# Kernel optimization log

Measured on AMD Instinct MI355X. Metric: run time of the kernel, lower is better.

Reference implementation:

```python
import jax, jax.numpy as jnp
import numpy as np

N_NODES = 100000
N_EDGES = 1600000
D_IN = 256
D_OUT = 128


def setup_inputs() -> dict:
    key = jax.random.key(0)
    k1, k2, k3, k4, k5 = jax.random.split(key, 5)
    x = jax.random.normal(k1, (N_NODES, D_IN), dtype=jnp.float32)
    # Glorot-uniform weight as in weight_variable_glorot
    init_range = np.sqrt(6.0 / (D_IN + D_OUT))
    W = jax.random.uniform(k2, (D_IN, D_OUT), dtype=jnp.float32,
                           minval=-init_range, maxval=init_range)
    adj_rows = jax.random.randint(k3, (N_EDGES,), 0, N_NODES, dtype=jnp.int32)
    adj_cols = jax.random.randint(k4, (N_EDGES,), 0, N_NODES, dtype=jnp.int32)
    adj_vals = jax.random.uniform(k5, (N_EDGES,), dtype=jnp.float32)
    return {"x": x, "W": W, "adj_rows": adj_rows, "adj_cols": adj_cols,
            "adj_vals": adj_vals}


def reference(x, W, adj_rows, adj_cols, adj_vals):
    # dropout with keep_prob = 1 - 0.0 is the identity -> omitted
    h = x @ W                                    # [N, D_OUT] dense projection
    # sparse (COO) adjacency @ h : out[r] += v * h[c]
    msgs = adj_vals[:, None] * h[adj_cols]       # [E, D_OUT]
    agg = jax.ops.segment_sum(msgs, adj_rows, num_segments=N_NODES)
    return jax.nn.relu(agg)                      # act = tf.nn.relu
```

## Files before the change

### kernel.cpp

```cpp
#include <hip/hip_runtime.h>
#include <hip/hip_bf16.h>

#define N_NODES 100000
#define N_EDGES 1600000
#define D_IN 256
#define D_OUT 128

typedef short bf16x8 __attribute__((ext_vector_type(8)));
typedef float f32x4 __attribute__((ext_vector_type(4)));

__device__ __forceinline__ unsigned short f2bf(float f) {
    unsigned int u = __builtin_bit_cast(unsigned int, f);
    u += 0x7fffu + ((u >> 16) & 1u);
    return (unsigned short)(u >> 16);
}
__device__ __forceinline__ float bf_lo(unsigned int h) {
    return __builtin_bit_cast(float, h << 16);
}
__device__ __forceinline__ float bf_hi(unsigned int h) {
    return __builtin_bit_cast(float, h & 0xffff0000u);
}

__global__ __launch_bounds__(256) void convert_w(const float* __restrict__ W,
                                                 unsigned short* __restrict__ WbT) {
    int i = blockIdx.x * 256 + threadIdx.x;
    int k = i >> 7;
    int n = i & 127;
    WbT[(size_t)n * D_IN + k] = f2bf(W[i]);
}

__global__ __launch_bounds__(256) void gemm_mfma(const float* __restrict__ x,
                                                 const unsigned short* __restrict__ WbT,
                                                 unsigned short* __restrict__ hb) {
    const int wave = threadIdx.x >> 6;
    const int lane = threadIdx.x & 63;
    const int row0 = blockIdx.x * 128 + wave * 32;
    if (row0 >= N_NODES) return;
    const int m = lane & 15;
    const int q = lane >> 4;

    const float* xr0 = x + (size_t)(row0 + m) * D_IN;
    const float* xr1 = x + (size_t)(row0 + 16 + m) * D_IN;

    f32x4 acc[2][8];
#pragma unroll
    for (int h = 0; h < 2; ++h)
#pragma unroll
        for (int nt = 0; nt < 8; ++nt) acc[h][nt] = (f32x4){0.f, 0.f, 0.f, 0.f};

#pragma unroll
    for (int kc = 0; kc < 8; ++kc) {
        const int kb = kc * 32 + q * 8;
        float4 a00 = *(const float4*)(xr0 + kb);
        float4 a01 = *(const float4*)(xr0 + kb + 4);
        float4 a10 = *(const float4*)(xr1 + kb);
        float4 a11 = *(const float4*)(xr1 + kb + 4);
        bf16x8 af0, af1;
        af0[0] = (short)f2bf(a00.x); af0[1] = (short)f2bf(a00.y);
        af0[2] = (short)f2bf(a00.z); af0[3] = (short)f2bf(a00.w);
        af0[4] = (short)f2bf(a01.x); af0[5] = (short)f2bf(a01.y);
        af0[6] = (short)f2bf(a01.z); af0[7] = (short)f2bf(a01.w);
        af1[0] = (short)f2bf(a10.x); af1[1] = (short)f2bf(a10.y);
        af1[2] = (short)f2bf(a10.z); af1[3] = (short)f2bf(a10.w);
        af1[4] = (short)f2bf(a11.x); af1[5] = (short)f2bf(a11.y);
        af1[6] = (short)f2bf(a11.z); af1[7] = (short)f2bf(a11.w);
#pragma unroll
        for (int nt = 0; nt < 8; ++nt) {
            bf16x8 bf = *(const bf16x8*)(WbT + (size_t)(nt * 16 + m) * D_IN + kb);
            acc[0][nt] = __builtin_amdgcn_mfma_f32_16x16x32_bf16(af0, bf, acc[0][nt], 0, 0, 0);
            acc[1][nt] = __builtin_amdgcn_mfma_f32_16x16x32_bf16(af1, bf, acc[1][nt], 0, 0, 0);
        }
    }

#pragma unroll
    for (int h = 0; h < 2; ++h)
#pragma unroll
        for (int nt = 0; nt < 8; ++nt)
#pragma unroll
            for (int r = 0; r < 4; ++r) {
                int grow = row0 + h * 16 + q * 4 + r;
                hb[(size_t)grow * D_OUT + nt * 16 + m] = f2bf(acc[h][nt][r]);
            }
}

__global__ __launch_bounds__(256) void hist_rows(const int* __restrict__ rows,
                                                 int* __restrict__ counts) {
    int i = blockIdx.x * 256 + threadIdx.x;
    if (i < N_EDGES / 4) {
        int4 r = *(const int4*)(rows + i * 4);
        atomicAdd(&counts[r.x], 1);
        atomicAdd(&counts[r.y], 1);
        atomicAdd(&counts[r.z], 1);
        atomicAdd(&counts[r.w], 1);
    }
}

#define SCHUNK 1024
__global__ __launch_bounds__(1024) void scan_reduce(const int* __restrict__ counts,
                                                    int* __restrict__ bsum, int n) {
    __shared__ int ws[16];
    const int t = threadIdx.x, lane = t & 63, wid = t >> 6;
    int i = blockIdx.x * SCHUNK + t;
    int v = (i < n) ? counts[i] : 0;
#pragma unroll
    for (int off = 32; off >= 1; off >>= 1) v += __shfl_down(v, off);
    if (lane == 0) ws[wid] = v;
    __syncthreads();
    if (t == 0) {
        int s = 0;
#pragma unroll
        for (int w = 0; w < 16; ++w) s += ws[w];
        bsum[blockIdx.x] = s;
    }
}

__global__ __launch_bounds__(64) void scan_bsums(int* __restrict__ bsum, int nb) {
    const int lane = threadIdx.x;
    int carry = 0;
    for (int base = 0; base < nb; base += 64) {
        int i = base + lane;
        int v = (i < nb) ? bsum[i] : 0;
        int x = v;
#pragma unroll
        for (int off = 1; off < 64; off <<= 1) {
            int u = __shfl_up(x, off);
            if (lane >= off) x += u;
        }
        if (i < nb) bsum[i] = x - v + carry;
        carry += __shfl(x, 63);
    }
}

__global__ __launch_bounds__(1024) void scan_apply(const int* __restrict__ counts,
                                                   const int* __restrict__ bsum,
                                                   int* __restrict__ ptr,
                                                   int* __restrict__ cursor, int n) {
    __shared__ int wtot[16];
    const int t = threadIdx.x, lane = t & 63, wid = t >> 6;
    int i = blockIdx.x * SCHUNK + t;
    int v = (i < n) ? counts[i] : 0;
    int x = v;
#pragma unroll
    for (int off = 1; off < 64; off <<= 1) {
        int u = __shfl_up(x, off);
        if (lane >= off) x += u;
    }
    if (lane == 63) wtot[wid] = x;
    __syncthreads();
    if (wid == 0) {
        int wv = (lane < 16) ? wtot[lane] : 0;
        int y = wv;
#pragma unroll
        for (int off = 1; off < 16; off <<= 1) {
            int u = __shfl_up(y, off);
            if (lane >= off) y += u;
        }
        if (lane < 16) wtot[lane] = y - wv;
    }
    __syncthreads();
    int excl = (x - v) + wtot[wid] + bsum[blockIdx.x];
    if (i < n) {
        ptr[i] = excl;
        cursor[i] = excl;
        if (i == n - 1) ptr[n] = excl + v;
    }
}

#define NWIN 8
#define ROWS_PER_WIN (N_NODES / NWIN)
#define PERM_SLICES 125
__global__ __launch_bounds__(256) void permute_edges(const int* __restrict__ rows,
                                                     const int* __restrict__ cols,
                                                     const float* __restrict__ vals,
                                                     int* __restrict__ cursor,
                                                     int2* __restrict__ edge_r) {
    const int w     = blockIdx.x & (NWIN - 1);
    const int slice = blockIdx.x >> 3;
    const int lo = w * ROWS_PER_WIN;
    const int hi = lo + ROWS_PER_WIN;
    const int per = (N_EDGES / 4) / PERM_SLICES;
    const int beg = slice * per;
    const int end = beg + per;
    for (int i = beg + (int)threadIdx.x; i < end; i += 256) {
        int4   r = *((const int4*)rows + i);
        int4   c = *((const int4*)cols + i);
        float4 v = *((const float4*)vals + i);
        if (r.x >= lo && r.x < hi) {
            int p = atomicAdd(&cursor[r.x], 1);
            edge_r[p] = make_int2(c.x, __builtin_bit_cast(int, v.x));
        }
        if (r.y >= lo && r.y < hi) {
            int p = atomicAdd(&cursor[r.y], 1);
            edge_r[p] = make_int2(c.y, __builtin_bit_cast(int, v.y));
        }
        if (r.z >= lo && r.z < hi) {
            int p = atomicAdd(&cursor[r.z], 1);
            edge_r[p] = make_int2(c.z, __builtin_bit_cast(int, v.z));
        }
        if (r.w >= lo && r.w < hi) {
            int p = atomicAdd(&cursor[r.w], 1);
            edge_r[p] = make_int2(c.w, __builtin_bit_cast(int, v.w));
        }
    }
}

__global__ __launch_bounds__(256) void gather_rows(const int* __restrict__ ptr,
                                                   const int2* __restrict__ edge_r,
                                                   const unsigned short* __restrict__ hb,
                                                   float* __restrict__ out) {
    int row  = blockIdx.x * 4 + (threadIdx.x >> 6);
    int lane = threadIdx.x & 63;
    if (row >= N_NODES) return;
    int beg = __builtin_amdgcn_readfirstlane(ptr[row]);
    int end = __builtin_amdgcn_readfirstlane(ptr[row + 1]);

    float ax0 = 0.f, ay0 = 0.f, ax1 = 0.f, ay1 = 0.f;
    float ax2 = 0.f, ay2 = 0.f, ax3 = 0.f, ay3 = 0.f;
    int j = beg;
    for (; j + 4 <= end; j += 4) {
        int2 e0 = edge_r[j + 0];
        int2 e1 = edge_r[j + 1];
        int2 e2 = edge_r[j + 2];
        int2 e3 = edge_r[j + 3];
        unsigned int h0 = *(const unsigned int*)(hb + (size_t)e0.x * D_OUT + lane * 2);
        unsigned int h1 = *(const unsigned int*)(hb + (size_t)e1.x * D_OUT + lane * 2);
        unsigned int h2 = *(const unsigned int*)(hb + (size_t)e2.x * D_OUT + lane * 2);
        unsigned int h3 = *(const unsigned int*)(hb + (size_t)e3.x * D_OUT + lane * 2);
        float v0 = __builtin_bit_cast(float, e0.y);
        float v1 = __builtin_bit_cast(float, e1.y);
        float v2 = __builtin_bit_cast(float, e2.y);
        float v3 = __builtin_bit_cast(float, e3.y);
        ax0 = fmaf(v0, bf_lo(h0), ax0); ay0 = fmaf(v0, bf_hi(h0), ay0);
        ax1 = fmaf(v1, bf_lo(h1), ax1); ay1 = fmaf(v1, bf_hi(h1), ay1);
        ax2 = fmaf(v2, bf_lo(h2), ax2); ay2 = fmaf(v2, bf_hi(h2), ay2);
        ax3 = fmaf(v3, bf_lo(h3), ax3); ay3 = fmaf(v3, bf_hi(h3), ay3);
    }
    for (; j < end; ++j) {
        int2 e = edge_r[j];
        unsigned int h = *(const unsigned int*)(hb + (size_t)e.x * D_OUT + lane * 2);
        float v = __builtin_bit_cast(float, e.y);
        ax0 = fmaf(v, bf_lo(h), ax0);
        ay0 = fmaf(v, bf_hi(h), ay0);
    }
    float accx = (ax0 + ax1) + (ax2 + ax3);
    float accy = (ay0 + ay1) + (ay2 + ay3);
    float2 o = make_float2(fmaxf(accx, 0.f), fmaxf(accy, 0.f));
    *(float2*)(out + (size_t)row * D_OUT + lane * 2) = o;
}

extern "C" void kernel_launch(void* const* d_in, const int* in_sizes, int n_in,
                              void* d_out, int out_size, void* d_ws, size_t ws_size,
                              hipStream_t stream) {
    const float* x    = (const float*)d_in[0];
    const float* W    = (const float*)d_in[1];
    const int*   rows = (const int*)d_in[2];
    const int*   cols = (const int*)d_in[3];
    const float* vals = (const float*)d_in[4];
    float* out = (float*)d_out;

    char* ws = (char*)d_ws;
    size_t off = 0;
    unsigned short* hb  = (unsigned short*)(ws + off); off += ((size_t)N_NODES * D_OUT * 2 + 255) & ~(size_t)255;
    unsigned short* WbT = (unsigned short*)(ws + off); off += ((size_t)D_IN * D_OUT * 2 + 255) & ~(size_t)255;
    int*  ptr    = (int*)(ws + off); off += ((size_t)(N_NODES + 1) * 4 + 255) & ~(size_t)255;
    int*  cursor = (int*)(ws + off); off += ((size_t)N_NODES * 4 + 255) & ~(size_t)255;
    int2* edge_r = (int2*)(ws + off); off += ((size_t)N_EDGES * 8 + 255) & ~(size_t)255;
    int*  bsum   = (int*)(ws + off); off += 4096;

    const int nscan = (N_NODES + SCHUNK - 1) / SCHUNK;

    convert_w<<<(D_IN * D_OUT) / 256, 256, 0, stream>>>(W, WbT);
    gemm_mfma<<<(N_NODES + 127) / 128, 256, 0, stream>>>(x, WbT, hb);

    (void)hipMemsetAsync(cursor, 0, (size_t)N_NODES * 4, stream);
    hist_rows<<<(N_EDGES / 4 + 255) / 256, 256, 0, stream>>>(rows, cursor);
    scan_reduce<<<nscan, 1024, 0, stream>>>(cursor, bsum, N_NODES);
    scan_bsums<<<1, 64, 0, stream>>>(bsum, nscan);
    scan_apply<<<nscan, 1024, 0, stream>>>(cursor, bsum, ptr, cursor, N_NODES);
    permute_edges<<<NWIN * PERM_SLICES, 256, 0, stream>>>(rows, cols, vals, cursor, edge_r);

    gather_rows<<<(N_NODES + 3) / 4, 256, 0, stream>>>(ptr, edge_r, hb, out);
}
```

Measured before the change: 419.7 us.

## Fuse histogram into GEMM launch, fold memset and block-sum scan into neighbors

Zeroing of the cursor array moves into the weight-conversion kernel. The row histogram becomes extra blocks of the GEMM launch so both run concurrently, and the block-sum scan is recomputed redundantly in every scan_apply block. Together these remove a memset and two kernel launches. permute_edges now uses twice as many slices and loads cols/vals only for edges that fall in its window, trading vector loads for scattered scalar loads in exchange for less wasted read traffic.

```diff
diff --git a/kernel.cpp b/kernel.cpp
--- a/kernel.cpp
+++ b/kernel.cpp
@@ -22,16 +22,35 @@
 }
 
 __global__ __launch_bounds__(256) void convert_w(const float* __restrict__ W,
-                                                 unsigned short* __restrict__ WbT) {
+                                                 unsigned short* __restrict__ WbT,
+                                                 int* __restrict__ cursor) {
     int i = blockIdx.x * 256 + threadIdx.x;
     int k = i >> 7;
     int n = i & 127;
     WbT[(size_t)n * D_IN + k] = f2bf(W[i]);
-}
-
-__global__ __launch_bounds__(256) void gemm_mfma(const float* __restrict__ x,
+    int z = i * 4;
+    if (z < N_NODES) *(int4*)(cursor + z) = make_int4(0, 0, 0, 0);
+}
+
+#define GEMM_BLOCKS ((N_NODES + 127) / 128)
+#define HIST_BLOCKS ((N_EDGES / 4 + 255) / 256)
+__global__ __launch_bounds__(256) void gemm_hist(const float* __restrict__ x,
                                                  const unsigned short* __restrict__ WbT,
-                                                 unsigned short* __restrict__ hb) {
+                                                 unsigned short* __restrict__ hb,
+                                                 const int* __restrict__ rows,
+                                                 int* __restrict__ counts) {
+    if (blockIdx.x >= GEMM_BLOCKS) {
+        int i = (blockIdx.x - GEMM_BLOCKS) * 256 + threadIdx.x;
+        if (i < N_EDGES / 4) {
+            int4 r = *(const int4*)(rows + i * 4);
+            atomicAdd(&counts[r.x], 1);
+            atomicAdd(&counts[r.y], 1);
+            atomicAdd(&counts[r.z], 1);
+            atomicAdd(&counts[r.w], 1);
+        }
+        return;
+    }
+
     const int wave = threadIdx.x >> 6;
     const int lane = threadIdx.x & 63;
     const int row0 = blockIdx.x * 128 + wave * 32;
@@ -83,19 +102,8 @@
             }
 }
 
-__global__ __launch_bounds__(256) void hist_rows(const int* __restrict__ rows,
-                                                 int* __restrict__ counts) {
-    int i = blockIdx.x * 256 + threadIdx.x;
-    if (i < N_EDGES / 4) {
-        int4 r = *(const int4*)(rows + i * 4);
-        atomicAdd(&counts[r.x], 1);
-        atomicAdd(&counts[r.y], 1);
-        atomicAdd(&counts[r.z], 1);
-        atomicAdd(&counts[r.w], 1);
-    }
-}
-
 #define SCHUNK 1024
+#define NSCAN ((N_NODES + SCHUNK - 1) / SCHUNK)
 __global__ __launch_bounds__(1024) void scan_reduce(const int* __restrict__ counts,
                                                     int* __restrict__ bsum, int n) {
     __shared__ int ws[16];
@@ -114,28 +122,12 @@
     }
 }
 
-__global__ __launch_bounds__(64) void scan_bsums(int* __restrict__ bsum, int nb) {
-    const int lane = threadIdx.x;
-    int carry = 0;
-    for (int base = 0; base < nb; base += 64) {
-        int i = base + lane;
-        int v = (i < nb) ? bsum[i] : 0;
-        int x = v;
-#pragma unroll
-        for (int off = 1; off < 64; off <<= 1) {
-            int u = __shfl_up(x, off);
-            if (lane >= off) x += u;
-        }
-        if (i < nb) bsum[i] = x - v + carry;
-        carry += __shfl(x, 63);
-    }
-}
-
 __global__ __launch_bounds__(1024) void scan_apply(const int* __restrict__ counts,
                                                    const int* __restrict__ bsum,
                                                    int* __restrict__ ptr,
-                                                   int* __restrict__ cursor, int n) {
+                                                   int* __restrict__ cursor, int n, int nb) {
     __shared__ int wtot[16];
+    __shared__ int bpre[128];
     const int t = threadIdx.x, lane = t & 63, wid = t >> 6;
     int i = blockIdx.x * SCHUNK + t;
     int v = (i < n) ? counts[i] : 0;
@@ -146,6 +138,22 @@
         if (lane >= off) x += u;
     }
     if (lane == 63) wtot[wid] = x;
+
+    if (wid == 0) {
+        int carry = 0;
+        for (int base = 0; base < nb; base += 64) {
+            int idx = base + lane;
+            int bv = (idx < nb) ? bsum[idx] : 0;
+            int bx = bv;
+#pragma unroll
+            for (int off = 1; off < 64; off <<= 1) {
+                int u = __shfl_up(bx, off);
+                if (lane >= off) bx += u;
+            }
+            if (idx < nb) bpre[idx] = bx - bv + carry;
+            carry += __shfl(bx, 63);
+        }
+    }
     __syncthreads();
     if (wid == 0) {
         int wv = (lane < 16) ? wtot[lane] : 0;
@@ -158,7 +166,7 @@
         if (lane < 16) wtot[lane] = y - wv;
     }
     __syncthreads();
-    int excl = (x - v) + wtot[wid] + bsum[blockIdx.x];
+    int excl = (x - v) + wtot[wid] + bpre[blockIdx.x];
     if (i < n) {
         ptr[i] = excl;
         cursor[i] = excl;
@@ -168,7 +176,7 @@
 
 #define NWIN 8
 #define ROWS_PER_WIN (N_NODES / NWIN)
-#define PERM_SLICES 125
+#define PERM_SLICES 250
 __global__ __launch_bounds__(256) void permute_edges(const int* __restrict__ rows,
                                                      const int* __restrict__ cols,
                                                      const float* __restrict__ vals,
@@ -182,24 +190,23 @@
     const int beg = slice * per;
     const int end = beg + per;
     for (int i = beg + (int)threadIdx.x; i < end; i += 256) {
-        int4   r = *((const int4*)rows + i);
-        int4   c = *((const int4*)cols + i);
-        float4 v = *((const float4*)vals + i);
+        int4 r = *((const int4*)rows + i);
+        const int e = i * 4;
         if (r.x >= lo && r.x < hi) {
             int p = atomicAdd(&cursor[r.x], 1);
-            edge_r[p] = make_int2(c.x, __builtin_bit_cast(int, v.x));
+            edge_r[p] = make_int2(cols[e + 0], __builtin_bit_cast(int, vals[e + 0]));
         }
         if (r.y >= lo && r.y < hi) {
             int p = atomicAdd(&cursor[r.y], 1);
-            edge_r[p] = make_int2(c.y, __builtin_bit_cast(int, v.y));
+            edge_r[p] = make_int2(cols[e + 1], __builtin_bit_cast(int, vals[e + 1]));
         }
         if (r.z >= lo && r.z < hi) {
             int p = atomicAdd(&cursor[r.z], 1);
-            edge_r[p] = make_int2(c.z, __builtin_bit_cast(int, v.z));
+            edge_r[p] = make_int2(cols[e + 2], __builtin_bit_cast(int, vals[e + 2]));
         }
         if (r.w >= lo && r.w < hi) {
             int p = atomicAdd(&cursor[r.w], 1);
-            edge_r[p] = make_int2(c.w, __builtin_bit_cast(int, v.w));
+            edge_r[p] = make_int2(cols[e + 3], __builtin_bit_cast(int, vals[e + 3]));
         }
     }
 }
@@ -267,17 +274,10 @@
     int2* edge_r = (int2*)(ws + off); off += ((size_t)N_EDGES * 8 + 255) & ~(size_t)255;
     int*  bsum   = (int*)(ws + off); off += 4096;
 
-    const int nscan = (N_NODES + SCHUNK - 1) / SCHUNK;
-
-    convert_w<<<(D_IN * D_OUT) / 256, 256, 0, stream>>>(W, WbT);
-    gemm_mfma<<<(N_NODES + 127) / 128, 256, 0, stream>>>(x, WbT, hb);
-
-    (void)hipMemsetAsync(cursor, 0, (size_t)N_NODES * 4, stream);
-    hist_rows<<<(N_EDGES / 4 + 255) / 256, 256, 0, stream>>>(rows, cursor);
-    scan_reduce<<<nscan, 1024, 0, stream>>>(cursor, bsum, N_NODES);
-    scan_bsums<<<1, 64, 0, stream>>>(bsum, nscan);
-    scan_apply<<<nscan, 1024, 0, stream>>>(cursor, bsum, ptr, cursor, N_NODES);
+    convert_w<<<(D_IN * D_OUT) / 256, 256, 0, stream>>>(W, WbT, cursor);
+    gemm_hist<<<GEMM_BLOCKS + HIST_BLOCKS, 256, 0, stream>>>(x, WbT, hb, rows, cursor);
+    scan_reduce<<<NSCAN, 1024, 0, stream>>>(cursor, bsum, N_NODES);
+    scan_apply<<<NSCAN, 1024, 0, stream>>>(cursor, bsum, ptr, cursor, N_NODES, NSCAN);
     permute_edges<<<NWIN * PERM_SLICES, 256, 0, stream>>>(rows, cols, vals, cursor, edge_r);
-
     gather_rows<<<(N_NODES + 3) / 4, 256, 0, stream>>>(ptr, edge_r, hb, out);
 }
```

Measured after the change: 412.3 us. No clear change (-1.8%).
